# Performance work log

Measured on AMD Instinct MI355X. Metric: run time of the kernel, lower is better.

## Reference

```python
import jax, jax.numpy as jnp
import numpy as np

N_NODES = 100000
N_EDGES = 1600000
D = 128
L = 3


def setup_inputs() -> dict:
    key = jax.random.key(0)
    k1, k2, k3 = jax.random.split(key, 3)
    edge_index = jax.random.randint(k1, (2, N_EDGES), 0, N_NODES, dtype=jnp.int64)
    emb = jax.random.normal(k2, (N_NODES, D), dtype=jnp.float32)
    # Glorot-style scale for the per-layer linear weights
    Ws = jax.random.normal(k3, (L, D, D), dtype=jnp.float32) * (1.0 / np.sqrt(D))
    bs = jnp.zeros((L, D), dtype=jnp.float32)
    return {"edge_index": edge_index, "emb": emb, "Ws": Ws, "bs": bs}


def _gcn_forward(emb, Ws, bs, edge_index):
    n = emb.shape[0]
    self_loop = jnp.arange(n, dtype=edge_index.dtype)
    # PyG GCNConv adds self-loops and uses symmetric normalization
    row = jnp.concatenate([edge_index[0], self_loop])  # source nodes
    col = jnp.concatenate([edge_index[1], self_loop])  # target nodes
    deg = jax.ops.segment_sum(jnp.ones(row.shape[0], dtype=emb.dtype), col, num_segments=n)
    deg_inv_sqrt = jnp.where(deg > 0, jax.lax.rsqrt(jnp.maximum(deg, 1.0)), 0.0)
    norm = deg_inv_sqrt[row] * deg_inv_sqrt[col]  # [E+N]

    x = emb
    for l in range(Ws.shape[0]):
        h = x @ Ws[l]                              # [N, D] linear transform
        msg = h[row] * norm[:, None]               # gather + scale [E+N, D]
        x = jax.ops.segment_sum(msg, col, num_segments=n) + bs[l]  # scatter-add
        x = jax.nn.relu(x)                         # dropout is identity in eval
    return x


def reference(edge_index, emb, Ws, bs) -> jnp.ndarray:
    return _gcn_forward(emb, Ws, bs, edge_index)
```

## Files before the change

kernel.cpp:

```cpp
#include <hip/hip_runtime.h>
#include <hip/hip_fp16.h>
#include <cstdint>
#include <cstddef>

#define N_NODES 100000
#define N_PAD 100096
#define N_EDGES 1600000
#define D 128
#define NLAYERS 3
#define NB 3125
#define NBLK_E 128
#define EPB 12500
#define ENT_CAP 1024

typedef float f2v __attribute__((ext_vector_type(2)));
typedef float f4v __attribute__((ext_vector_type(4)));


__global__ __launch_bounds__(512) void hist1_kernel(const int* __restrict__ col,
                                                    int* __restrict__ hmat) {
    __shared__ int hist[NB];
    int b = blockIdx.x, t = threadIdx.x;
    for (int j = t; j < NB; j += 512) hist[j] = 0;
    __syncthreads();
    int base = b * EPB;
    for (int i = t; i < EPB; i += 512) {
        int c = col[base + i];
        atomicAdd(&hist[c >> 5], 1);
    }
    __syncthreads();
    for (int j = t; j < NB; j += 512) hmat[b * NB + j] = hist[j];
}

__global__ void btot_kernel(const int* __restrict__ hmat, int* __restrict__ btot) {
    int j = blockIdx.x * 256 + threadIdx.x;
    if (j < NB) {
        int s = 0;
        for (int b = 0; b < NBLK_E; b++) s += hmat[b * NB + j];
        btot[j] = s;
    }
}

__global__ void bscan_kernel(const int* __restrict__ btot, int* __restrict__ bstart, int nb, int e) {
    __shared__ int lsum[1024];
    int t = threadIdx.x;
    int vals[4];
    int v0 = 0;
#pragma unroll
    for (int j = 0; j < 4; j++) {
        int idx = t * 4 + j;
        int c = (idx < nb) ? btot[idx] : 0;
        vals[j] = c;
        v0 += c;
    }
    lsum[t] = v0;
    __syncthreads();
    for (int off = 1; off < 1024; off <<= 1) {
        int x = (t >= off) ? lsum[t - off] : 0;
        __syncthreads();
        lsum[t] += x;
        __syncthreads();
    }
    int base = lsum[t] - v0;
#pragma unroll
    for (int j = 0; j < 4; j++) {
        int idx = t * 4 + j;
        if (idx < nb) {
            bstart[idx] = base;
            base += vals[j];
        }
    }
    if (t == 0) bstart[nb] = e;
}

__global__ void hoff_kernel(const int* __restrict__ hmat, const int* __restrict__ bstart,
                            int* __restrict__ hoff) {
    int j = blockIdx.x * 256 + threadIdx.x;
    if (j < NB) {
        int run = bstart[j];
        for (int b = 0; b < NBLK_E; b++) {
            hoff[b * NB + j] = run;
            run += hmat[b * NB + j];
        }
    }
}

__global__ __launch_bounds__(512) void scatter_kernel(const int* __restrict__ row,
                                                      const int* __restrict__ col,
                                                      const int* __restrict__ hoff,
                                                      unsigned* __restrict__ bucketbuf) {
    __shared__ int cur[NB];
    int b = blockIdx.x, t = threadIdx.x;
    for (int j = t; j < NB; j += 512) cur[j] = hoff[b * NB + j];
    __syncthreads();
    int base = b * EPB;
    for (int i = t; i < EPB; i += 512) {
        int r = row[base + i], c = col[base + i];
        int pos = atomicAdd(&cur[c >> 5], 1);
        bucketbuf[pos] = ((unsigned)r << 5) | (unsigned)(c & 31);
    }
}

__global__ void fill2_kernel(const unsigned* __restrict__ bucketbuf, const int* __restrict__ bstart,
                             int* __restrict__ offsets, float* __restrict__ dinv,
                             int* __restrict__ src, int n, int e) {
    __shared__ unsigned ent[ENT_CAP];
    __shared__ int hist[32];
    __shared__ int cur[32];
    __shared__ int loff[32];
    int b = blockIdx.x, t = threadIdx.x;
    int s0 = bstart[b];
    int cnt = bstart[b + 1] - s0;
    if (cnt > ENT_CAP) cnt = ENT_CAP;
    if (t < 32) hist[t] = 0;
    __syncthreads();
    for (int i = t; i < cnt; i += 256) {
        unsigned v = bucketbuf[s0 + i];
        ent[i] = v;
        atomicAdd(&hist[v & 31], 1);
    }
    __syncthreads();
    if (t == 0) {
        int run = s0;
#pragma unroll
        for (int j = 0; j < 32; j++) {
            loff[j] = run;
            run += hist[j];
        }
    }
    __syncthreads();
    if (t < 32) {
        int node = b * 32 + t;
        int o = loff[t];
        offsets[node] = o;
        cur[t] = o;
        dinv[node] = rsqrtf((float)(hist[t] + 1));
    }
    if (b == 0 && t == 0) offsets[n] = e;
    __syncthreads();
    for (int i = t; i < cnt; i += 256) {
        unsigned v = ent[i];
        int pos = atomicAdd(&cur[v & 31], 1);
        src[pos] = (int)(v >> 5);
    }
}


__global__ void cast_kernel(const float2* __restrict__ in, const float* __restrict__ dinv,
                            __half2* __restrict__ out, int n2) {
    int i = blockIdx.x * 256 + threadIdx.x;
    if (i < n2) {
        float d = dinv[i >> 6];
        float2 v = in[i];
        out[i] = __floats2half2_rn(d * v.x, d * v.y);
    }
}

__global__ void agg_kernel(const __half2* __restrict__ xs, const int* __restrict__ offs,
                           float* __restrict__ out, const float* __restrict__ dinv,
                           const int* __restrict__ src) {
    int v = blockIdx.x;
    int f = threadIdx.x;
    float dv = dinv[v];
    float2 a0 = __half22float2(xs[(size_t)v * 64 + f]);
    float ax = a0.x;
    float ay = a0.y;
    int i = offs[v], s1 = offs[v + 1];
    for (; i + 7 < s1; i += 8) {
        int s[8];
#pragma unroll
        for (int j = 0; j < 8; j++) s[j] = src[i + j];
        float2 x[8];
#pragma unroll
        for (int j = 0; j < 8; j++) x[j] = __half22float2(xs[(size_t)s[j] * 64 + f]);
#pragma unroll
        for (int j = 0; j < 8; j++) {
            ax += x[j].x;
            ay += x[j].y;
        }
    }
    if (i < s1) {
        int last = s1 - 1;
        int s[8];
        float m[8];
#pragma unroll
        for (int j = 0; j < 8; j++) {
            int idx = i + j;
            bool in = idx < s1;
            s[j] = src[in ? idx : last];
            m[j] = in ? 1.0f : 0.0f;
        }
        float2 x[8];
#pragma unroll
        for (int j = 0; j < 8; j++) x[j] = __half22float2(xs[(size_t)s[j] * 64 + f]);
#pragma unroll
        for (int j = 0; j < 8; j++) {
            ax += m[j] * x[j].x;
            ay += m[j] * x[j].y;
        }
    }
    f2v r;
    r.x = dv * ax;
    r.y = dv * ay;
    __builtin_nontemporal_store(r, (f2v*)out + (size_t)v * 64 + f);
}

__global__ __launch_bounds__(256) void gemm_bias_relu_kernel(
    const float* __restrict__ A, const float* __restrict__ W,
    const float* __restrict__ bias, float* __restrict__ out,
    __half2* __restrict__ xs_out, const float* __restrict__ dinv,
    int write_h, int write_out, int n) {
    __shared__ float sA[32 * 128];
    __shared__ float sW[32 * 128];
    int t = threadIdx.x;
    int tx = t & 15;
    int ty = t >> 4;
    int row0 = blockIdx.x * 128;

    f4v acc[8][2];
#pragma unroll
    for (int r = 0; r < 8; r++) {
        acc[r][0] = (f4v){0.f, 0.f, 0.f, 0.f};
        acc[r][1] = (f4v){0.f, 0.f, 0.f, 0.f};
    }

    const f4v* A4 = (const f4v*)A;

    for (int kc = 0; kc < 4; kc++) {
        int kb = kc * 32;
        {
            const f4v* Wg = (const f4v*)(W + (size_t)kb * 128);
            f4v* sW4 = (f4v*)sW;
#pragma unroll
            for (int i = 0; i < 4; i++) sW4[t + 256 * i] = Wg[t + 256 * i];
        }
#pragma unroll
        for (int i = 0; i < 4; i++) {
            int idx = t + 256 * i;
            int r = idx >> 3;
            int q = idx & 7;
            f4v v = __builtin_nontemporal_load(&A4[(size_t)(row0 + r) * 32 + kc * 8 + q]);
            int k0 = q * 4;
            sA[(k0 + 0) * 128 + (r ^ ((k0 + 0) & 24))] = v.x;
            sA[(k0 + 1) * 128 + (r ^ ((k0 + 1) & 24))] = v.y;
            sA[(k0 + 2) * 128 + (r ^ ((k0 + 2) & 24))] = v.z;
            sA[(k0 + 3) * 128 + (r ^ ((k0 + 3) & 24))] = v.w;
        }
        __syncthreads();

#pragma unroll 8
        for (int k = 0; k < 32; k++) {
            const float* ap = &sA[k * 128 + ((ty * 8) ^ (k & 24))];
            f4v a0 = *(const f4v*)ap;
            f4v a1 = *(const f4v*)(ap + 4);
            const float* bp = &sW[k * 128 + tx * 8];
            f4v b0 = *(const f4v*)bp;
            f4v b1 = *(const f4v*)(bp + 4);
#pragma unroll
            for (int r = 0; r < 4; r++) {
                acc[r][0] += a0[r] * b0;
                acc[r][1] += a0[r] * b1;
                acc[r + 4][0] += a1[r] * b0;
                acc[r + 4][1] += a1[r] * b1;
            }
        }
        __syncthreads();
    }

    f4v bb0 = ((const f4v*)bias)[tx * 2];
    f4v bb1 = ((const f4v*)bias)[tx * 2 + 1];
#pragma unroll
    for (int r = 0; r < 8; r++) {
        int rowi = row0 + ty * 8 + r;
        if (rowi >= n) continue;
        f4v o0 = acc[r][0] + bb0;
        f4v o1 = acc[r][1] + bb1;
#pragma unroll
        for (int j = 0; j < 4; j++) {
            o0[j] = fmaxf(o0[j], 0.0f);
            o1[j] = fmaxf(o1[j], 0.0f);
        }
        if (write_out) {
            __builtin_nontemporal_store(o0, (f4v*)out + (size_t)rowi * 32 + tx * 2);
            __builtin_nontemporal_store(o1, (f4v*)out + (size_t)rowi * 32 + tx * 2 + 1);
        }
        if (write_h) {
            float dr = dinv[rowi];
            __half2 h[4];
            h[0] = __floats2half2_rn(dr * o0[0], dr * o0[1]);
            h[1] = __floats2half2_rn(dr * o0[2], dr * o0[3]);
            h[2] = __floats2half2_rn(dr * o1[0], dr * o1[1]);
            h[3] = __floats2half2_rn(dr * o1[2], dr * o1[3]);
            *(uint4*)&xs_out[(size_t)rowi * 64 + tx * 4] = *(uint4*)h;
        }
    }
}


extern "C" void kernel_launch(void* const* d_in, const int* in_sizes, int n_in,
                              void* d_out, int out_size, void* d_ws, size_t ws_size,
                              hipStream_t stream) {
    const int* edge = (const int*)d_in[0];
    const float* emb = (const float*)d_in[1];
    const float* Ws = (const float*)d_in[2];
    const float* bs = (const float*)d_in[3];
    float* out = (float*)d_out;

    const int n = N_NODES, e = N_EDGES;
    const int* row = edge;
    const int* col = edge + e;

    char* p = (char*)d_ws;
    float* aggbuf = (float*)p;
    int* hmat = (int*)p;
    int* hoff = hmat + (size_t)NBLK_E * NB;
    p += (size_t)N_PAD * D * 4;
    __half2* xs = (__half2*)p;
    unsigned* bucketbuf = (unsigned*)p;
    p += (size_t)n * D * 2;
    int* csr_src  = (int*)p;    p += (size_t)e * 4;
    float* dinv   = (float*)p;  p += (size_t)n * 4;
    int* offsets  = (int*)p;    p += (size_t)(n + 1) * 4;
    int* btot     = (int*)p;    p += (size_t)NB * 4;
    int* bstart   = (int*)p;    p += (size_t)(NB + 1) * 4;

    hist1_kernel<<<NBLK_E, 512, 0, stream>>>(col, hmat);
    btot_kernel<<<(NB + 255) / 256, 256, 0, stream>>>(hmat, btot);
    bscan_kernel<<<1, 1024, 0, stream>>>(btot, bstart, NB, e);
    hoff_kernel<<<(NB + 255) / 256, 256, 0, stream>>>(hmat, bstart, hoff);
    scatter_kernel<<<NBLK_E, 512, 0, stream>>>(row, col, hoff, bucketbuf);
    fill2_kernel<<<NB, 256, 0, stream>>>(bucketbuf, bstart, offsets, dinv, csr_src, n, e);

    int n2 = n * 64;
    cast_kernel<<<(n2 + 255) / 256, 256, 0, stream>>>((const float2*)emb, dinv, xs, n2);

    const int ngb = N_PAD / 128;
    for (int l = 0; l < NLAYERS; l++) {
        agg_kernel<<<n, 64, 0, stream>>>(xs, offsets, aggbuf, dinv, csr_src);
        gemm_bias_relu_kernel<<<ngb, 256, 0, stream>>>(
            aggbuf, Ws + (size_t)l * D * D, bs + (size_t)l * D, out,
            xs, dinv,
            (l < NLAYERS - 1) ? 1 : 0, (l == NLAYERS - 1) ? 1 : 0, n);
    }
}
```

Measured before the change: 525.5 us.

## Replace FP32 SIMT GEMM with split-FP16 MFMA GEMM using hi/lo operands

The dense per-layer transform now runs on MFMA 16x16x32 f16 instructions instead of FP32 FMAs. Accuracy is kept with a three-term split: both the aggregated activations and the weights are stored as fp16 high and low parts. The aggregation kernel writes two fp16 buffers instead of one fp32 buffer, and a new kernel pre-splits and transposes the weights. The GEMM also prefetches the next K chunk into registers while computing the current one. The cost is three MFMAs per product, an extra launch, and a narrower output store pattern in the epilogue.

```diff
diff --git a/kernel.cpp b/kernel.cpp
--- a/kernel.cpp
+++ b/kernel.cpp
@@ -15,6 +15,9 @@
 
 typedef float f2v __attribute__((ext_vector_type(2)));
 typedef float f4v __attribute__((ext_vector_type(4)));
+typedef _Float16 f16x8 __attribute__((ext_vector_type(8)));
+typedef float f32x4 __attribute__((ext_vector_type(4)));
+typedef unsigned u32x4 __attribute__((ext_vector_type(4)));
 
 
 __global__ __launch_bounds__(512) void hist1_kernel(const int* __restrict__ col,
@@ -156,9 +159,19 @@
     }
 }
 
+__global__ void wsplit_kernel(const float* __restrict__ W,
+                              _Float16* __restrict__ Wh, _Float16* __restrict__ Wl) {
+    int c = blockIdx.x, l = blockIdx.y, k = threadIdx.x;
+    float w = W[(size_t)l * 16384 + k * 128 + c];
+    _Float16 h = (_Float16)w;
+    float r = w - (float)h;
+    Wh[(size_t)l * 16384 + c * 128 + k] = h;
+    Wl[(size_t)l * 16384 + c * 128 + k] = (_Float16)r;
+}
+
 __global__ void agg_kernel(const __half2* __restrict__ xs, const int* __restrict__ offs,
-                           float* __restrict__ out, const float* __restrict__ dinv,
-                           const int* __restrict__ src) {
+                           unsigned* __restrict__ Ah, unsigned* __restrict__ Al,
+                           const float* __restrict__ dinv, const int* __restrict__ src) {
     int v = blockIdx.x;
     int f = threadIdx.x;
     float dv = dinv[v];
@@ -199,99 +212,114 @@
             ay += m[j] * x[j].y;
         }
     }
-    f2v r;
-    r.x = dv * ax;
-    r.y = dv * ay;
-    __builtin_nontemporal_store(r, (f2v*)out + (size_t)v * 64 + f);
-}
-
-__global__ __launch_bounds__(256) void gemm_bias_relu_kernel(
-    const float* __restrict__ A, const float* __restrict__ W,
+    float rx = dv * ax, ry = dv * ay;
+    __half2 h2 = __floats2half2_rn(rx, ry);
+    float2 hb = __half22float2(h2);
+    __half2 l2 = __floats2half2_rn(rx - hb.x, ry - hb.y);
+    __builtin_nontemporal_store(__builtin_bit_cast(unsigned, h2), Ah + (size_t)v * 64 + f);
+    __builtin_nontemporal_store(__builtin_bit_cast(unsigned, l2), Al + (size_t)v * 64 + f);
+}
+
+__global__ __launch_bounds__(256) void gemm_mfma_kernel(
+    const _Float16* __restrict__ Ahp, const _Float16* __restrict__ Alp,
+    const _Float16* __restrict__ Whp, const _Float16* __restrict__ Wlp,
     const float* __restrict__ bias, float* __restrict__ out,
     __half2* __restrict__ xs_out, const float* __restrict__ dinv,
-    int write_h, int write_out, int n) {
-    __shared__ float sA[32 * 128];
-    __shared__ float sW[32 * 128];
+    int write_h, int write_out, int nrows) {
+    __shared__ _Float16 sA[2][128][40];
+    __shared__ _Float16 sW[2][128][40];
     int t = threadIdx.x;
-    int tx = t & 15;
-    int ty = t >> 4;
+    int lane = t & 63, wv = t >> 6;
+    int lrow = lane & 15, kg = lane >> 4;
     int row0 = blockIdx.x * 128;
 
-    f4v acc[8][2];
-#pragma unroll
-    for (int r = 0; r < 8; r++) {
-        acc[r][0] = (f4v){0.f, 0.f, 0.f, 0.f};
-        acc[r][1] = (f4v){0.f, 0.f, 0.f, 0.f};
-    }
-
-    const f4v* A4 = (const f4v*)A;
-
+    f32x4 acc[2][8];
+#pragma unroll
+    for (int m = 0; m < 2; m++)
+#pragma unroll
+        for (int nn = 0; nn < 8; nn++) acc[m][nn] = (f32x4){0.f, 0.f, 0.f, 0.f};
+
+    const u32x4* Aq[2] = {(const u32x4*)Ahp, (const u32x4*)Alp};
+    const u32x4* Wq[2] = {(const u32x4*)Whp, (const u32x4*)Wlp};
+
+    u32x4 av[4], wvr[4];
+
+#define LOADCH(kc)                                                                    \
+    {                                                                                 \
+        _Pragma("unroll") for (int i = 0; i < 4; i++) {                               \
+            int sid = t + 256 * i;                                                    \
+            int p = i >> 1;                                                           \
+            int rr = (sid >> 2) & 127;                                                \
+            int k2 = sid & 3;                                                         \
+            av[i] = __builtin_nontemporal_load(                                       \
+                &Aq[p][(size_t)(row0 + rr) * 16 + (kc) * 4 + k2]);                    \
+            wvr[i] = Wq[p][(size_t)rr * 16 + (kc) * 4 + k2];                          \
+        }                                                                             \
+    }
+
+#define STORECH()                                                                     \
+    {                                                                                 \
+        _Pragma("unroll") for (int i = 0; i < 4; i++) {                               \
+            int sid = t + 256 * i;                                                    \
+            int p = i >> 1;                                                           \
+            int rr = (sid >> 2) & 127;                                                \
+            int k2 = sid & 3;                                                         \
+            *(u32x4*)&sA[p][rr][k2 * 8] = av[i];                                      \
+            *(u32x4*)&sW[p][rr][k2 * 8] = wvr[i];                                     \
+        }                                                                             \
+    }
+
+    LOADCH(0);
+#pragma unroll
     for (int kc = 0; kc < 4; kc++) {
-        int kb = kc * 32;
-        {
-            const f4v* Wg = (const f4v*)(W + (size_t)kb * 128);
-            f4v* sW4 = (f4v*)sW;
-#pragma unroll
-            for (int i = 0; i < 4; i++) sW4[t + 256 * i] = Wg[t + 256 * i];
-        }
-#pragma unroll
-        for (int i = 0; i < 4; i++) {
-            int idx = t + 256 * i;
-            int r = idx >> 3;
-            int q = idx & 7;
-            f4v v = __builtin_nontemporal_load(&A4[(size_t)(row0 + r) * 32 + kc * 8 + q]);
-            int k0 = q * 4;
-            sA[(k0 + 0) * 128 + (r ^ ((k0 + 0) & 24))] = v.x;
-            sA[(k0 + 1) * 128 + (r ^ ((k0 + 1) & 24))] = v.y;
-            sA[(k0 + 2) * 128 + (r ^ ((k0 + 2) & 24))] = v.z;
-            sA[(k0 + 3) * 128 + (r ^ ((k0 + 3) & 24))] = v.w;
-        }
         __syncthreads();
-
-#pragma unroll 8
-        for (int k = 0; k < 32; k++) {
-            const float* ap = &sA[k * 128 + ((ty * 8) ^ (k & 24))];
-            f4v a0 = *(const f4v*)ap;
-            f4v a1 = *(const f4v*)(ap + 4);
-            const float* bp = &sW[k * 128 + tx * 8];
-            f4v b0 = *(const f4v*)bp;
-            f4v b1 = *(const f4v*)(bp + 4);
-#pragma unroll
-            for (int r = 0; r < 4; r++) {
-                acc[r][0] += a0[r] * b0;
-                acc[r][1] += a0[r] * b1;
-                acc[r + 4][0] += a1[r] * b0;
-                acc[r + 4][1] += a1[r] * b1;
+        STORECH();
+        if (kc < 3) LOADCH(kc + 1);
+        __syncthreads();
+
+        f16x8 a0h = *(const f16x8*)&sA[0][wv * 32 + lrow][kg * 8];
+        f16x8 a1h = *(const f16x8*)&sA[0][wv * 32 + 16 + lrow][kg * 8];
+        f16x8 a0l = *(const f16x8*)&sA[1][wv * 32 + lrow][kg * 8];
+        f16x8 a1l = *(const f16x8*)&sA[1][wv * 32 + 16 + lrow][kg * 8];
+#pragma unroll
+        for (int nn = 0; nn < 8; nn++) {
+            f16x8 bh = *(const f16x8*)&sW[0][nn * 16 + lrow][kg * 8];
+            f16x8 bl = *(const f16x8*)&sW[1][nn * 16 + lrow][kg * 8];
+            acc[0][nn] = __builtin_amdgcn_mfma_f32_16x16x32_f16(a0h, bh, acc[0][nn], 0, 0, 0);
+            acc[0][nn] = __builtin_amdgcn_mfma_f32_16x16x32_f16(a0l, bh, acc[0][nn], 0, 0, 0);
+            acc[0][nn] = __builtin_amdgcn_mfma_f32_16x16x32_f16(a0h, bl, acc[0][nn], 0, 0, 0);
+            acc[1][nn] = __builtin_amdgcn_mfma_f32_16x16x32_f16(a1h, bh, acc[1][nn], 0, 0, 0);
+            acc[1][nn] = __builtin_amdgcn_mfma_f32_16x16x32_f16(a1l, bh, acc[1][nn], 0, 0, 0);
+            acc[1][nn] = __builtin_amdgcn_mfma_f32_16x16x32_f16(a1h, bl, acc[1][nn], 0, 0, 0);
+        }
+    }
+#undef LOADCH
+#undef STORECH
+
+    float bcolv[8];
+#pragma unroll
+    for (int nn = 0; nn < 8; nn++) bcolv[nn] = bias[nn * 16 + lrow];
+#pragma unroll
+    for (int m = 0; m < 2; m++) {
+        int rbase = row0 + wv * 32 + m * 16 + kg * 4;
+#pragma unroll
+        for (int j = 0; j < 4; j++) {
+            int rowi = rbase + j;
+            bool ok = rowi < nrows;
+            float dvr = (ok && write_h) ? dinv[rowi] : 0.f;
+#pragma unroll
+            for (int nn = 0; nn < 8; nn++) {
+                float o = fmaxf(acc[m][nn][j] + bcolv[nn], 0.f);
+                float o2 = __shfl_xor(o, 1);
+                int col = nn * 16 + lrow;
+                if (ok) {
+                    if (write_out)
+                        __builtin_nontemporal_store(o, out + (size_t)rowi * 128 + col);
+                    if (write_h && !(lane & 1))
+                        xs_out[(size_t)rowi * 64 + (col >> 1)] =
+                            __floats2half2_rn(dvr * o, dvr * o2);
+                }
             }
-        }
-        __syncthreads();
-    }
-
-    f4v bb0 = ((const f4v*)bias)[tx * 2];
-    f4v bb1 = ((const f4v*)bias)[tx * 2 + 1];
-#pragma unroll
-    for (int r = 0; r < 8; r++) {
-        int rowi = row0 + ty * 8 + r;
-        if (rowi >= n) continue;
-        f4v o0 = acc[r][0] + bb0;
-        f4v o1 = acc[r][1] + bb1;
-#pragma unroll
-        for (int j = 0; j < 4; j++) {
-            o0[j] = fmaxf(o0[j], 0.0f);
-            o1[j] = fmaxf(o1[j], 0.0f);
-        }
-        if (write_out) {
-            __builtin_nontemporal_store(o0, (f4v*)out + (size_t)rowi * 32 + tx * 2);
-            __builtin_nontemporal_store(o1, (f4v*)out + (size_t)rowi * 32 + tx * 2 + 1);
-        }
-        if (write_h) {
-            float dr = dinv[rowi];
-            __half2 h[4];
-            h[0] = __floats2half2_rn(dr * o0[0], dr * o0[1]);
-            h[1] = __floats2half2_rn(dr * o0[2], dr * o0[3]);
-            h[2] = __floats2half2_rn(dr * o1[0], dr * o1[1]);
-            h[3] = __floats2half2_rn(dr * o1[2], dr * o1[3]);
-            *(uint4*)&xs_out[(size_t)rowi * 64 + tx * 4] = *(uint4*)h;
         }
     }
 }
@@ -311,10 +339,12 @@
     const int* col = edge + e;
 
     char* p = (char*)d_ws;
-    float* aggbuf = (float*)p;
+    _Float16* Ah = (_Float16*)p;
     int* hmat = (int*)p;
     int* hoff = hmat + (size_t)NBLK_E * NB;
-    p += (size_t)N_PAD * D * 4;
+    p += (size_t)N_PAD * D * 2;
+    _Float16* Al = (_Float16*)p;
+    p += (size_t)N_PAD * D * 2;
     __half2* xs = (__half2*)p;
     unsigned* bucketbuf = (unsigned*)p;
     p += (size_t)n * D * 2;
@@ -323,6 +353,8 @@
     int* offsets  = (int*)p;    p += (size_t)(n + 1) * 4;
     int* btot     = (int*)p;    p += (size_t)NB * 4;
     int* bstart   = (int*)p;    p += (size_t)(NB + 1) * 4;
+    _Float16* WhT = (_Float16*)p; p += (size_t)NLAYERS * D * D * 2;
+    _Float16* WlT = (_Float16*)p; p += (size_t)NLAYERS * D * D * 2;
 
     hist1_kernel<<<NBLK_E, 512, 0, stream>>>(col, hmat);
     btot_kernel<<<(NB + 255) / 256, 256, 0, stream>>>(hmat, btot);
@@ -330,16 +362,18 @@
     hoff_kernel<<<(NB + 255) / 256, 256, 0, stream>>>(hmat, bstart, hoff);
     scatter_kernel<<<NBLK_E, 512, 0, stream>>>(row, col, hoff, bucketbuf);
     fill2_kernel<<<NB, 256, 0, stream>>>(bucketbuf, bstart, offsets, dinv, csr_src, n, e);
+    wsplit_kernel<<<dim3(128, NLAYERS), 128, 0, stream>>>(Ws, WhT, WlT);
 
     int n2 = n * 64;
     cast_kernel<<<(n2 + 255) / 256, 256, 0, stream>>>((const float2*)emb, dinv, xs, n2);
 
     const int ngb = N_PAD / 128;
     for (int l = 0; l < NLAYERS; l++) {
-        agg_kernel<<<n, 64, 0, stream>>>(xs, offsets, aggbuf, dinv, csr_src);
-        gemm_bias_relu_kernel<<<ngb, 256, 0, stream>>>(
-            aggbuf, Ws + (size_t)l * D * D, bs + (size_t)l * D, out,
-            xs, dinv,
+        agg_kernel<<<n, 64, 0, stream>>>(xs, offsets, (unsigned*)Ah, (unsigned*)Al,
+                                         dinv, csr_src);
+        gemm_mfma_kernel<<<ngb, 256, 0, stream>>>(
+            Ah, Al, WhT + (size_t)l * D * D, WlT + (size_t)l * D * D,
+            bs + (size_t)l * D, out, xs, dinv,
             (l < NLAYERS - 1) ? 1 : 0, (l == NLAYERS - 1) ? 1 : 0, n);
     }
 }
```

Result: faster. 493.7 us (-6.1%).
